# Performance work log

Hardware: AMD Instinct MI355X
Metric: run time of the kernel (lower is better)

Reference implementation:

```python
import jax, jax.numpy as jnp
import numpy as np

H = 2048          # hidden_size
IM = 1024         # moe_intermediate_size
E = 16            # n_routed_experts
K = 8             # num_experts_per_tok
N_SHARED = 2      # n_shared_experts
IS = IM * N_SHARED  # shared expert intermediate
B, L = 1, 2048
SCALE = 2.5       # routed_scaling_factor
W_INIT = 0.02


def setup_inputs() -> dict:
    key = jax.random.key(0)
    ks = jax.random.split(key, 9)
    return {
        "hidden_states": jax.random.normal(ks[0], (B, L, H), jnp.float32),
        "gate_w": jax.random.normal(ks[1], (E, H), jnp.float32) * W_INIT,
        "Wg": jax.random.normal(ks[2], (E, H, IM), jnp.float32) * W_INIT,
        "Wu": jax.random.normal(ks[3], (E, H, IM), jnp.float32) * W_INIT,
        "Wd": jax.random.normal(ks[4], (E, IM, H), jnp.float32) * W_INIT,
        "sWg": jax.random.normal(ks[5], (H, IS), jnp.float32) * W_INIT,
        "sWu": jax.random.normal(ks[6], (H, IS), jnp.float32) * W_INIT,
        "sWd": jax.random.normal(ks[7], (IS, H), jnp.float32) * W_INIT,
    }


def reference(hidden_states, gate_w, Wg, Wu, Wd, sWg, sWu, sWd):
    orig_shape = hidden_states.shape
    h = hidden_states.reshape(-1, H)                      # [T, H]
    T = h.shape[0]

    # shared expert (SwiGLU MLP)
    shared = (jax.nn.silu(h @ sWg) * (h @ sWu)) @ sWd     # [T, H]

    # sigmoid router + top-k gating
    router_logits = h @ gate_w.T                          # [T, E]
    routing_weights = jax.nn.sigmoid(router_logits)
    topk_w, topk_idx = jax.lax.top_k(routing_weights, K)  # [T, K]
    topk_w = topk_w / (jnp.sum(topk_w, axis=-1, keepdims=True) + 1e-6)
    topk_w = topk_w * SCALE

    # dense [T, E] combine weights (zero for unselected experts)
    comb = jnp.zeros((T, E), h.dtype).at[jnp.arange(T)[:, None], topk_idx].add(topk_w)

    # all-expert SwiGLU MLP (batched over experts), then weighted combine
    g = jnp.einsum("th,ehi->eti", h, Wg)                  # [E, T, IM]
    u = jnp.einsum("th,ehi->eti", h, Wu)
    eo = jnp.einsum("eti,eih->eth", jax.nn.silu(g) * u, Wd)  # [E, T, H]
    routed = jnp.einsum("eth,te->th", eo, comb)           # [T, H]

    return (shared + routed).reshape(orig_shape)
```

## Files before the change

kernel.cpp:

```cpp
#include <hip/hip_runtime.h>
#include <hip/hip_bf16.h>
#include <stdint.h>

#define H_DIM  2048
#define IM_DIM 1024
#define E_NUM  16
#define TOPK   8
#define IS_DIM 2048
#define SCALE_F 2.5f

#define BM 128
#define BN 128
#define BK 32
#define LDSP 40

typedef __attribute__((ext_vector_type(8))) short   short8;
typedef __attribute__((ext_vector_type(8))) __bf16  bf16x8;
typedef __attribute__((ext_vector_type(4))) float   float4v;
typedef unsigned short ushort_t;

#define GLOAD_LDS16(gp, lp) \
    __builtin_amdgcn_global_load_lds((__attribute__((address_space(1))) void*)(gp), \
                                     (__attribute__((address_space(3))) void*)(lp), 16, 0, 0)

static __device__ __forceinline__ ushort_t f2bf(float x) {
    union { float f; uint32_t u; } v; v.f = x;
    uint32_t r = v.u + 0x7fffu + ((v.u >> 16) & 1u);
    return (ushort_t)(r >> 16);
}

__global__ void cast_h_kernel(const float* __restrict__ h, ushort_t* __restrict__ hb, int n4) {
    int i = blockIdx.x * blockDim.x + threadIdx.x;
    if (i < n4) {
        float4 v = ((const float4*)h)[i];
        ushort4 o;
        o.x = f2bf(v.x); o.y = f2bf(v.y); o.z = f2bf(v.z); o.w = f2bf(v.w);
        ((ushort4*)hb)[i] = o;
    }
}

__global__ void router_kernel(const float* __restrict__ h, const float* __restrict__ gw,
                              float* __restrict__ comb, int T) {
    int t = blockIdx.x;
    int l = threadIdx.x;
    const float* hr = h + (size_t)t * H_DIM;
    __shared__ float logits[E_NUM];
    for (int e = 0; e < E_NUM; e++) {
        const float* g = gw + e * H_DIM;
        float p = 0.f;
        #pragma unroll 8
        for (int j = l; j < H_DIM; j += 64) p += hr[j] * g[j];
        #pragma unroll
        for (int off = 32; off > 0; off >>= 1) p += __shfl_down(p, off);
        if (l == 0) logits[e] = p;
    }
    __syncthreads();
    if (l == 0) {
        float sig[E_NUM]; bool sel[E_NUM];
        #pragma unroll
        for (int e = 0; e < E_NUM; e++) { sig[e] = 1.f / (1.f + expf(-logits[e])); sel[e] = false; }
        #pragma unroll
        for (int k = 0; k < TOPK; k++) {
            int bi = 0; float bv = -1.f;
            #pragma unroll
            for (int e = 0; e < E_NUM; e++)
                if (!sel[e] && sig[e] > bv) { bv = sig[e]; bi = e; }
            sel[bi] = true;
        }
        float s = 0.f;
        #pragma unroll
        for (int e = 0; e < E_NUM; e++) if (sel[e]) s += sig[e];
        float inv = SCALE_F / (s + 1e-6f);
        #pragma unroll
        for (int e = 0; e < E_NUM; e++)
            comb[(size_t)t * E_NUM + e] = sel[e] ? sig[e] * inv : 0.f;
    }
}

__global__ __launch_bounds__(256)
void transpose_cvt_kernel(const float* __restrict__ src, ushort_t* __restrict__ dst,
                          int K, int N, size_t sStride, size_t dStride)
{
    __shared__ float tile[64 * 65];
    int z = blockIdx.z;
    const float* S = src + (size_t)z * sStride;
    ushort_t* D = dst + (size_t)z * dStride;
    int k0 = blockIdx.x * 64, n0 = blockIdx.y * 64;
    int tid = threadIdx.x;
    int tr = tid >> 4, tc = (tid & 15) * 4;
    #pragma unroll
    for (int p = 0; p < 4; p++) {
        int r = tr + 16 * p;
        float4 v = *(const float4*)&S[(size_t)(k0 + r) * N + n0 + tc];
        tile[(tc + 0) * 65 + r] = v.x;
        tile[(tc + 1) * 65 + r] = v.y;
        tile[(tc + 2) * 65 + r] = v.z;
        tile[(tc + 3) * 65 + r] = v.w;
    }
    __syncthreads();
    #pragma unroll
    for (int p = 0; p < 4; p++) {
        int n = tr + 16 * p;
        ushort4 o;
        o.x = f2bf(tile[n * 65 + tc + 0]);
        o.y = f2bf(tile[n * 65 + tc + 1]);
        o.z = f2bf(tile[n * 65 + tc + 2]);
        o.w = f2bf(tile[n * 65 + tc + 3]);
        *(ushort4*)&D[(size_t)(n0 + n) * K + k0 + tc] = o;
    }
}


__global__ __launch_bounds__(256, 2)
void gemm1f_kernel(const ushort_t* __restrict__ A, int lda,
                   const ushort_t* __restrict__ Bg0, const ushort_t* __restrict__ Bu0,
                   size_t bSeg,
                   ushort_t* __restrict__ C0, size_t cSeg, int ldc,
                   const float* __restrict__ comb, int Kdim)
{
    __shared__ ushort_t Als[BM * BK];
    __shared__ ushort_t Bgs[BN * BK];
    __shared__ ushort_t Bus[BN * BK];

    int z = blockIdx.z;
    const ushort_t* Bg = Bg0 + (size_t)z * bSeg;
    const ushort_t* Bu = Bu0 + (size_t)z * bSeg;
    ushort_t* C = C0 + (size_t)z * cSeg;
    int t0 = blockIdx.x * BM, n0 = blockIdx.y * BN;
    int tid = threadIdx.x, lane = tid & 63, wid = tid >> 6;
    int wm = (wid & 1) * 64, wn = (wid >> 1) * 64;
    int quad = lane >> 4, l15 = lane & 15;

    int srow = lane >> 2;
    int scol = (lane & 3) * 8;
    int rb = wid * 32;

    float4v accg[4][4], accu[4][4];
    #pragma unroll
    for (int i = 0; i < 4; i++)
        #pragma unroll
        for (int j = 0; j < 4; j++) {
            accg[i][j] = (float4v){0.f, 0.f, 0.f, 0.f};
            accu[i][j] = (float4v){0.f, 0.f, 0.f, 0.f};
        }

    const ushort_t* Ab0  = A  + (size_t)(t0 + rb + srow)      * lda  + scol;
    const ushort_t* Ab1  = A  + (size_t)(t0 + rb + 16 + srow) * lda  + scol;
    const ushort_t* Bgb0 = Bg + (size_t)(n0 + rb + srow)      * Kdim + scol;
    const ushort_t* Bgb1 = Bg + (size_t)(n0 + rb + 16 + srow) * Kdim + scol;
    const ushort_t* Bub0 = Bu + (size_t)(n0 + rb + srow)      * Kdim + scol;
    const ushort_t* Bub1 = Bu + (size_t)(n0 + rb + 16 + srow) * Kdim + scol;
    ushort_t* lA0  = &Als[rb * BK];
    ushort_t* lA1  = &Als[(rb + 16) * BK];
    ushort_t* lBg0 = &Bgs[rb * BK];
    ushort_t* lBg1 = &Bgs[(rb + 16) * BK];
    ushort_t* lBu0 = &Bus[rb * BK];
    ushort_t* lBu1 = &Bus[(rb + 16) * BK];

    for (int k0 = 0; k0 < Kdim; k0 += BK) {
        GLOAD_LDS16(Ab0 + k0,  lA0);
        GLOAD_LDS16(Ab1 + k0,  lA1);
        GLOAD_LDS16(Bgb0 + k0, lBg0);
        GLOAD_LDS16(Bgb1 + k0, lBg1);
        GLOAD_LDS16(Bub0 + k0, lBu0);
        GLOAD_LDS16(Bub1 + k0, lBu1);
        __syncthreads();

        bf16x8 af[4], bg[4], bu[4];
        #pragma unroll
        for (int i = 0; i < 4; i++)
            af[i] = *(const bf16x8*)&Als[(wm + i * 16 + l15) * BK + quad * 8];
        #pragma unroll
        for (int j = 0; j < 4; j++) {
            bg[j] = *(const bf16x8*)&Bgs[(wn + j * 16 + l15) * BK + quad * 8];
            bu[j] = *(const bf16x8*)&Bus[(wn + j * 16 + l15) * BK + quad * 8];
        }
        #pragma unroll
        for (int i = 0; i < 4; i++)
            #pragma unroll
            for (int j = 0; j < 4; j++) {
                accg[i][j] = __builtin_amdgcn_mfma_f32_16x16x32_bf16(af[i], bg[j], accg[i][j], 0, 0, 0);
                accu[i][j] = __builtin_amdgcn_mfma_f32_16x16x32_bf16(af[i], bu[j], accu[i][j], 0, 0, 0);
            }
        __syncthreads();
    }

    #pragma unroll
    for (int i = 0; i < 4; i++) {
        #pragma unroll
        for (int r = 0; r < 4; r++) {
            int t = t0 + wm + i * 16 + quad * 4 + r;
            float sc = comb ? comb[(size_t)t * E_NUM + z] : 1.f;
            #pragma unroll
            for (int j = 0; j < 4; j++) {
                float g = accg[i][j][r], u = accu[i][j][r];
                float sg = g / (1.f + __expf(-g));
                float v = sg * u * sc;
                int c = n0 + wn + j * 16 + l15;
                C[(size_t)t * ldc + c] = f2bf(v);
            }
        }
    }
}

__global__ __launch_bounds__(256, 2)
void gemm2f_kernel(const ushort_t* __restrict__ A0, size_t aSeg, int lda,
                   const ushort_t* __restrict__ B0, size_t bSeg,
                   float* __restrict__ Out, int N,
                   int nsegPerZ, int Kper, int mode)
{
    __shared__ ushort_t Als[BM * BK];
    __shared__ ushort_t Bls[BN * BK];

    int t0 = blockIdx.x * BM, n0 = blockIdx.y * BN;
    int z = blockIdx.z;
    int tid = threadIdx.x, lane = tid & 63, wid = tid >> 6;
    int wm = (wid & 1) * 64, wn = (wid >> 1) * 64;
    int quad = lane >> 4, l15 = lane & 15;

    int srow = lane >> 2;
    int scol = (lane & 3) * 8;
    int rb = wid * 32;

    float4v acc[4][4];
    #pragma unroll
    for (int i = 0; i < 4; i++)
        #pragma unroll
        for (int j = 0; j < 4; j++) acc[i][j] = (float4v){0.f, 0.f, 0.f, 0.f};

    ushort_t* lA0 = &Als[rb * BK];
    ushort_t* lA1 = &Als[(rb + 16) * BK];
    ushort_t* lB0 = &Bls[rb * BK];
    ushort_t* lB1 = &Bls[(rb + 16) * BK];

    for (int s = 0; s < nsegPerZ; s++) {
        int seg = z * nsegPerZ + s;
        const ushort_t* A = A0 + (size_t)seg * aSeg;
        const ushort_t* B = B0 + (size_t)seg * bSeg;
        const ushort_t* Ab0 = A + (size_t)(t0 + rb + srow)      * lda  + scol;
        const ushort_t* Ab1 = A + (size_t)(t0 + rb + 16 + srow) * lda  + scol;
        const ushort_t* Bb0 = B + (size_t)(n0 + rb + srow)      * Kper + scol;
        const ushort_t* Bb1 = B + (size_t)(n0 + rb + 16 + srow) * Kper + scol;

        for (int k0 = 0; k0 < Kper; k0 += BK) {
            GLOAD_LDS16(Ab0 + k0, lA0);
            GLOAD_LDS16(Ab1 + k0, lA1);
            GLOAD_LDS16(Bb0 + k0, lB0);
            GLOAD_LDS16(Bb1 + k0, lB1);
            __syncthreads();

            bf16x8 af[4], bf[4];
            #pragma unroll
            for (int i = 0; i < 4; i++)
                af[i] = *(const bf16x8*)&Als[(wm + i * 16 + l15) * BK + quad * 8];
            #pragma unroll
            for (int j = 0; j < 4; j++)
                bf[j] = *(const bf16x8*)&Bls[(wn + j * 16 + l15) * BK + quad * 8];
            #pragma unroll
            for (int i = 0; i < 4; i++)
                #pragma unroll
                for (int j = 0; j < 4; j++)
                    acc[i][j] = __builtin_amdgcn_mfma_f32_16x16x32_bf16(af[i], bf[j], acc[i][j], 0, 0, 0);
            __syncthreads();
        }
    }

    #pragma unroll
    for (int i = 0; i < 4; i++) {
        #pragma unroll
        for (int r = 0; r < 4; r++) {
            int t = t0 + wm + i * 16 + quad * 4 + r;
            #pragma unroll
            for (int j = 0; j < 4; j++) {
                int c = n0 + wn + j * 16 + l15;
                size_t idx = (size_t)t * N + c;
                float v = acc[i][j][r];
                if (mode == 0) Out[idx] = v;
                else if (mode == 1) Out[idx] += v;
                else atomicAdd(&Out[idx], v);
            }
        }
    }
}


__global__ __launch_bounds__(256)
void gemm1_kernel(const ushort_t* __restrict__ A, int lda,
                  const float* __restrict__ Bg0, const float* __restrict__ Bu0,
                  size_t bSeg, int ldb,
                  ushort_t* __restrict__ C0, size_t cSeg, int ldc,
                  const float* __restrict__ comb, int Kdim)
{
    __shared__ ushort_t Als[BM * LDSP];
    __shared__ ushort_t Bgs[BN * LDSP];
    __shared__ ushort_t Bus[BN * LDSP];

    int z = blockIdx.z;
    const float* Bg = Bg0 + (size_t)z * bSeg;
    const float* Bu = Bu0 + (size_t)z * bSeg;
    ushort_t* C = C0 + (size_t)z * cSeg;

    int t0 = blockIdx.x * BM;
    int n0 = blockIdx.y * BN;
    int tid = threadIdx.x;
    int lane = tid & 63, wid = tid >> 6;
    int wm = (wid & 1) * 64, wn = (wid >> 1) * 64;
    int quad = lane >> 4, l15 = lane & 15;

    float4v accg[4][4], accu[4][4];
    #pragma unroll
    for (int i = 0; i < 4; i++)
        #pragma unroll
        for (int j = 0; j < 4; j++) {
            accg[i][j] = (float4v){0.f, 0.f, 0.f, 0.f};
            accu[i][j] = (float4v){0.f, 0.f, 0.f, 0.f};
        }

    int a_r  = tid >> 2, a_oc = tid & 3;
    int b_ko = (tid >> 4) & 3;
    int b_n  = 2 * ((tid & 15) + ((tid >> 6) << 4));

    for (int k0 = 0; k0 < Kdim; k0 += BK) {
        __syncthreads();
        {
            const ushort_t* s0 = A + (size_t)(t0 + a_r) * lda + k0 + a_oc * 8;
            *(short8*)&Als[a_r * LDSP + a_oc * 8] = *(const short8*)s0;
            const ushort_t* s1 = A + (size_t)(t0 + a_r + 64) * lda + k0 + a_oc * 8;
            *(short8*)&Als[(a_r + 64) * LDSP + a_oc * 8] = *(const short8*)s1;
        }
        {
            short8 g0, g1, u0, u1;
            #pragma unroll
            for (int j = 0; j < 8; j++) {
                size_t roff = (size_t)(k0 + b_ko * 8 + j) * ldb + n0 + b_n;
                float2 vg = *(const float2*)&Bg[roff];
                float2 vu = *(const float2*)&Bu[roff];
                g0[j] = (short)f2bf(vg.x); g1[j] = (short)f2bf(vg.y);
                u0[j] = (short)f2bf(vu.x); u1[j] = (short)f2bf(vu.y);
            }
            *(short8*)&Bgs[b_n * LDSP + b_ko * 8]       = g0;
            *(short8*)&Bgs[(b_n + 1) * LDSP + b_ko * 8] = g1;
            *(short8*)&Bus[b_n * LDSP + b_ko * 8]       = u0;
            *(short8*)&Bus[(b_n + 1) * LDSP + b_ko * 8] = u1;
        }
        __syncthreads();

        bf16x8 af[4], bg[4], bu[4];
        #pragma unroll
        for (int i = 0; i < 4; i++)
            af[i] = *(const bf16x8*)&Als[(wm + i * 16 + l15) * LDSP + quad * 8];
        #pragma unroll
        for (int j = 0; j < 4; j++) {
            bg[j] = *(const bf16x8*)&Bgs[(wn + j * 16 + l15) * LDSP + quad * 8];
            bu[j] = *(const bf16x8*)&Bus[(wn + j * 16 + l15) * LDSP + quad * 8];
        }
        #pragma unroll
        for (int i = 0; i < 4; i++)
            #pragma unroll
            for (int j = 0; j < 4; j++) {
                accg[i][j] = __builtin_amdgcn_mfma_f32_16x16x32_bf16(af[i], bg[j], accg[i][j], 0, 0, 0);
                accu[i][j] = __builtin_amdgcn_mfma_f32_16x16x32_bf16(af[i], bu[j], accu[i][j], 0, 0, 0);
            }
    }

    #pragma unroll
    for (int i = 0; i < 4; i++) {
        #pragma unroll
        for (int r = 0; r < 4; r++) {
            int t = t0 + wm + i * 16 + quad * 4 + r;
            float sc = comb ? comb[(size_t)t * E_NUM + z] : 1.f;
            #pragma unroll
            for (int j = 0; j < 4; j++) {
                float g = accg[i][j][r], u = accu[i][j][r];
                float sg = g / (1.f + __expf(-g));
                float v = sg * u * sc;
                int c = n0 + wn + j * 16 + l15;
                C[(size_t)t * ldc + c] = f2bf(v);
            }
        }
    }
}

__global__ __launch_bounds__(256)
void gemm2_kernel(const ushort_t* __restrict__ A0, size_t aSeg, int lda,
                  const float* __restrict__ B0, size_t bSeg, int ldb,
                  float* __restrict__ Out, int N,
                  int nseg, int Kper, int accum)
{
    __shared__ ushort_t Als[BM * LDSP];
    __shared__ ushort_t Bls[BN * LDSP];

    int t0 = blockIdx.x * BM;
    int n0 = blockIdx.y * BN;
    int tid = threadIdx.x;
    int lane = tid & 63, wid = tid >> 6;
    int wm = (wid & 1) * 64, wn = (wid >> 1) * 64;
    int quad = lane >> 4, l15 = lane & 15;

    float4v acc[4][4];
    #pragma unroll
    for (int i = 0; i < 4; i++)
        #pragma unroll
        for (int j = 0; j < 4; j++) acc[i][j] = (float4v){0.f, 0.f, 0.f, 0.f};

    int a_r  = tid >> 2, a_oc = tid & 3;
    int b_ko = (tid >> 4) & 3;
    int b_n  = 2 * ((tid & 15) + ((tid >> 6) << 4));

    for (int seg = 0; seg < nseg; seg++) {
        const ushort_t* A = A0 + (size_t)seg * aSeg;
        const float*    B = B0 + (size_t)seg * bSeg;
        for (int k0 = 0; k0 < Kper; k0 += BK) {
            __syncthreads();
            {
                const ushort_t* s0 = A + (size_t)(t0 + a_r) * lda + k0 + a_oc * 8;
                *(short8*)&Als[a_r * LDSP + a_oc * 8] = *(const short8*)s0;
                const ushort_t* s1 = A + (size_t)(t0 + a_r + 64) * lda + k0 + a_oc * 8;
                *(short8*)&Als[(a_r + 64) * LDSP + a_oc * 8] = *(const short8*)s1;
            }
            {
                short8 r0, r1;
                #pragma unroll
                for (int j = 0; j < 8; j++) {
                    size_t roff = (size_t)(k0 + b_ko * 8 + j) * ldb + n0 + b_n;
                    float2 v = *(const float2*)&B[roff];
                    r0[j] = (short)f2bf(v.x); r1[j] = (short)f2bf(v.y);
                }
                *(short8*)&Bls[b_n * LDSP + b_ko * 8]       = r0;
                *(short8*)&Bls[(b_n + 1) * LDSP + b_ko * 8] = r1;
            }
            __syncthreads();

            bf16x8 af[4], bf[4];
            #pragma unroll
            for (int i = 0; i < 4; i++)
                af[i] = *(const bf16x8*)&Als[(wm + i * 16 + l15) * LDSP + quad * 8];
            #pragma unroll
            for (int j = 0; j < 4; j++)
                bf[j] = *(const bf16x8*)&Bls[(wn + j * 16 + l15) * LDSP + quad * 8];
            #pragma unroll
            for (int i = 0; i < 4; i++)
                #pragma unroll
                for (int j = 0; j < 4; j++)
                    acc[i][j] = __builtin_amdgcn_mfma_f32_16x16x32_bf16(af[i], bf[j], acc[i][j], 0, 0, 0);
        }
    }

    #pragma unroll
    for (int i = 0; i < 4; i++) {
        #pragma unroll
        for (int r = 0; r < 4; r++) {
            int t = t0 + wm + i * 16 + quad * 4 + r;
            #pragma unroll
            for (int j = 0; j < 4; j++) {
                int c = n0 + wn + j * 16 + l15;
                size_t idx = (size_t)t * N + c;
                float v = acc[i][j][r];
                if (accum) Out[idx] += v; else Out[idx] = v;
            }
        }
    }
}


extern "C" void kernel_launch(void* const* d_in, const int* in_sizes, int n_in,
                              void* d_out, int out_size, void* d_ws, size_t ws_size,
                              hipStream_t stream) {
    const float* h      = (const float*)d_in[0];
    const float* gate_w = (const float*)d_in[1];
    const float* Wg     = (const float*)d_in[2];
    const float* Wu     = (const float*)d_in[3];
    const float* Wd     = (const float*)d_in[4];
    const float* sWg    = (const float*)d_in[5];
    const float* sWu    = (const float*)d_in[6];
    const float* sWd    = (const float*)d_in[7];
    float* out = (float*)d_out;
    int T = in_sizes[0] / H_DIM;
    (void)n_in; (void)out_size;

    char* ws = (char*)d_ws;
    size_t off = 0;
    auto alloc = [&](size_t bytes) -> void* {
        void* p = ws + off;
        off = (off + bytes + 255) & ~(size_t)255;
        return p;
    };
    ushort_t* h_bf  = (ushort_t*)alloc((size_t)T * H_DIM * 2);
    float*    comb  = (float*)   alloc((size_t)T * E_NUM * 4);
    ushort_t* act_s = (ushort_t*)alloc((size_t)T * IS_DIM * 2);
    ushort_t* act_r = (ushort_t*)alloc((size_t)E_NUM * T * IM_DIM * 2);
    ushort_t* bufS1 = (ushort_t*)alloc((size_t)IS_DIM * H_DIM * 2);
    ushort_t* bufS2 = (ushort_t*)alloc((size_t)IS_DIM * H_DIM * 2);
    ushort_t* bufW1 = (ushort_t*)alloc((size_t)E_NUM * IM_DIM * H_DIM * 2);
    ushort_t* bufW2 = (ushort_t*)alloc((size_t)E_NUM * IM_DIM * H_DIM * 2);
    size_t need = off;

    int n4 = T * H_DIM / 4;
    cast_h_kernel<<<(n4 + 255) / 256, 256, 0, stream>>>(h, h_bf, n4);
    router_kernel<<<T, 64, 0, stream>>>(h, gate_w, comb, T);

    if (ws_size >= need) {
        transpose_cvt_kernel<<<dim3(H_DIM / 64, IS_DIM / 64, 1), 256, 0, stream>>>(
            sWg, bufS1, H_DIM, IS_DIM, 0, 0);
        transpose_cvt_kernel<<<dim3(H_DIM / 64, IS_DIM / 64, 1), 256, 0, stream>>>(
            sWu, bufS2, H_DIM, IS_DIM, 0, 0);
        gemm1f_kernel<<<dim3(T / BM, IS_DIM / BN, 1), 256, 0, stream>>>(
            h_bf, H_DIM, bufS1, bufS2, 0, act_s, 0, IS_DIM, nullptr, H_DIM);

        transpose_cvt_kernel<<<dim3(H_DIM / 64, IM_DIM / 64, E_NUM), 256, 0, stream>>>(
            Wg, bufW1, H_DIM, IM_DIM, (size_t)H_DIM * IM_DIM, (size_t)IM_DIM * H_DIM);
        transpose_cvt_kernel<<<dim3(H_DIM / 64, IM_DIM / 64, E_NUM), 256, 0, stream>>>(
            Wu, bufW2, H_DIM, IM_DIM, (size_t)H_DIM * IM_DIM, (size_t)IM_DIM * H_DIM);
        gemm1f_kernel<<<dim3(T / BM, IM_DIM / BN, E_NUM), 256, 0, stream>>>(
            h_bf, H_DIM, bufW1, bufW2, (size_t)IM_DIM * H_DIM,
            act_r, (size_t)T * IM_DIM, IM_DIM, comb, H_DIM);

        transpose_cvt_kernel<<<dim3(IS_DIM / 64, H_DIM / 64, 1), 256, 0, stream>>>(
            sWd, bufS1, IS_DIM, H_DIM, 0, 0);
        gemm2f_kernel<<<dim3(T / BM, H_DIM / BN, 1), 256, 0, stream>>>(
            act_s, 0, IS_DIM, bufS1, 0, out, H_DIM, 1, IS_DIM, 0);

        transpose_cvt_kernel<<<dim3(IM_DIM / 64, H_DIM / 64, E_NUM), 256, 0, stream>>>(
            Wd, bufW1, IM_DIM, H_DIM, (size_t)IM_DIM * H_DIM, (size_t)H_DIM * IM_DIM);
        gemm2f_kernel<<<dim3(T / BM, H_DIM / BN, 2), 256, 0, stream>>>(
            act_r, (size_t)T * IM_DIM, IM_DIM, bufW1, (size_t)H_DIM * IM_DIM,
            out, H_DIM, E_NUM / 2, IM_DIM, 2);
    } else {
        gemm1_kernel<<<dim3(T / BM, IS_DIM / BN, 1), 256, 0, stream>>>(
            h_bf, H_DIM, sWg, sWu, 0, IS_DIM, act_s, 0, IS_DIM, nullptr, H_DIM);
        gemm1_kernel<<<dim3(T / BM, IM_DIM / BN, E_NUM), 256, 0, stream>>>(
            h_bf, H_DIM, Wg, Wu, (size_t)H_DIM * IM_DIM, IM_DIM,
            act_r, (size_t)T * IM_DIM, IM_DIM, comb, H_DIM);
        gemm2_kernel<<<dim3(T / BM, H_DIM / BN, 1), 256, 0, stream>>>(
            act_s, 0, IS_DIM, sWd, 0, H_DIM, out, H_DIM, 1, IS_DIM, 0);
        gemm2_kernel<<<dim3(T / BM, H_DIM / BN, 1), 256, 0, stream>>>(
            act_r, (size_t)T * IM_DIM, IM_DIM, Wd, (size_t)IM_DIM * H_DIM, H_DIM,
            out, H_DIM, E_NUM, IM_DIM, 1);
    }
}
```

Before: 1.149 ms.

## Replace dense all-expert MoE GEMMs with sparse gathered per-expert token lists

```diff
diff --git a/kernel.cpp b/kernel.cpp
--- a/kernel.cpp
+++ b/kernel.cpp
@@ -77,6 +77,37 @@
     }
 }
 
+__global__ void zero_cnt_kernel(int* __restrict__ cnt) {
+    if (threadIdx.x < E_NUM) cnt[threadIdx.x] = 0;
+}
+
+__global__ void build_lists_kernel(const float* __restrict__ comb, int* __restrict__ cnt,
+                                   int* __restrict__ idx, float* __restrict__ wv, int T) {
+    int t = blockIdx.x * blockDim.x + threadIdx.x;
+    if (t >= T) return;
+    #pragma unroll
+    for (int e = 0; e < E_NUM; e++) {
+        float w = comb[(size_t)t * E_NUM + e];
+        if (w != 0.f) {
+            int s = atomicAdd(&cnt[e], 1);
+            idx[(size_t)e * T + s] = t;
+            wv[(size_t)e * T + s] = w;
+        }
+    }
+}
+
+__global__ void pad_lists_kernel(const int* __restrict__ cnt, int* __restrict__ cntPad,
+                                 int* __restrict__ idx, float* __restrict__ wv, int T) {
+    int e = blockIdx.x;
+    int c = cnt[e];
+    int cp = (c + BM - 1) & ~(BM - 1);
+    if (threadIdx.x == 0) cntPad[e] = cp;
+    for (int s = c + threadIdx.x; s < cp; s += blockDim.x) {
+        idx[(size_t)e * T + s] = 0;
+        wv[(size_t)e * T + s] = 0.f;
+    }
+}
+
 __global__ __launch_bounds__(256)
 void transpose_cvt_kernel(const float* __restrict__ src, ushort_t* __restrict__ dst,
                           int K, int N, size_t sStride, size_t dStride)
@@ -113,27 +144,18 @@
 
 __global__ __launch_bounds__(256, 2)
 void gemm1f_kernel(const ushort_t* __restrict__ A, int lda,
-                   const ushort_t* __restrict__ Bg0, const ushort_t* __restrict__ Bu0,
-                   size_t bSeg,
-                   ushort_t* __restrict__ C0, size_t cSeg, int ldc,
-                   const float* __restrict__ comb, int Kdim)
+                   const ushort_t* __restrict__ Bg, const ushort_t* __restrict__ Bu,
+                   ushort_t* __restrict__ C, int ldc, int Kdim)
 {
     __shared__ ushort_t Als[BM * BK];
     __shared__ ushort_t Bgs[BN * BK];
     __shared__ ushort_t Bus[BN * BK];
 
-    int z = blockIdx.z;
-    const ushort_t* Bg = Bg0 + (size_t)z * bSeg;
-    const ushort_t* Bu = Bu0 + (size_t)z * bSeg;
-    ushort_t* C = C0 + (size_t)z * cSeg;
     int t0 = blockIdx.x * BM, n0 = blockIdx.y * BN;
     int tid = threadIdx.x, lane = tid & 63, wid = tid >> 6;
     int wm = (wid & 1) * 64, wn = (wid >> 1) * 64;
     int quad = lane >> 4, l15 = lane & 15;
-
-    int srow = lane >> 2;
-    int scol = (lane & 3) * 8;
-    int rb = wid * 32;
+    int srow = lane >> 2, scol = (lane & 3) * 8, rb = wid * 32;
 
     float4v accg[4][4], accu[4][4];
     #pragma unroll
@@ -190,37 +212,30 @@
         #pragma unroll
         for (int r = 0; r < 4; r++) {
             int t = t0 + wm + i * 16 + quad * 4 + r;
-            float sc = comb ? comb[(size_t)t * E_NUM + z] : 1.f;
             #pragma unroll
             for (int j = 0; j < 4; j++) {
                 float g = accg[i][j][r], u = accu[i][j][r];
                 float sg = g / (1.f + __expf(-g));
-                float v = sg * u * sc;
                 int c = n0 + wn + j * 16 + l15;
-                C[(size_t)t * ldc + c] = f2bf(v);
+                C[(size_t)t * ldc + c] = f2bf(sg * u);
             }
         }
     }
 }
 
 __global__ __launch_bounds__(256, 2)
-void gemm2f_kernel(const ushort_t* __restrict__ A0, size_t aSeg, int lda,
-                   const ushort_t* __restrict__ B0, size_t bSeg,
-                   float* __restrict__ Out, int N,
-                   int nsegPerZ, int Kper, int mode)
+void gemm2f_kernel(const ushort_t* __restrict__ A, int lda,
+                   const ushort_t* __restrict__ B,
+                   float* __restrict__ Out, int N, int Kper)
 {
     __shared__ ushort_t Als[BM * BK];
     __shared__ ushort_t Bls[BN * BK];
 
     int t0 = blockIdx.x * BM, n0 = blockIdx.y * BN;
-    int z = blockIdx.z;
     int tid = threadIdx.x, lane = tid & 63, wid = tid >> 6;
     int wm = (wid & 1) * 64, wn = (wid >> 1) * 64;
     int quad = lane >> 4, l15 = lane & 15;
-
-    int srow = lane >> 2;
-    int scol = (lane & 3) * 8;
-    int rb = wid * 32;
+    int srow = lane >> 2, scol = (lane & 3) * 8, rb = wid * 32;
 
     float4v acc[4][4];
     #pragma unroll
@@ -228,41 +243,35 @@
         #pragma unroll
         for (int j = 0; j < 4; j++) acc[i][j] = (float4v){0.f, 0.f, 0.f, 0.f};
 
+    const ushort_t* Ab0 = A + (size_t)(t0 + rb + srow)      * lda  + scol;
+    const ushort_t* Ab1 = A + (size_t)(t0 + rb + 16 + srow) * lda  + scol;
+    const ushort_t* Bb0 = B + (size_t)(n0 + rb + srow)      * Kper + scol;
+    const ushort_t* Bb1 = B + (size_t)(n0 + rb + 16 + srow) * Kper + scol;
     ushort_t* lA0 = &Als[rb * BK];
     ushort_t* lA1 = &Als[(rb + 16) * BK];
     ushort_t* lB0 = &Bls[rb * BK];
     ushort_t* lB1 = &Bls[(rb + 16) * BK];
 
-    for (int s = 0; s < nsegPerZ; s++) {
-        int seg = z * nsegPerZ + s;
-        const ushort_t* A = A0 + (size_t)seg * aSeg;
-        const ushort_t* B = B0 + (size_t)seg * bSeg;
-        const ushort_t* Ab0 = A + (size_t)(t0 + rb + srow)      * lda  + scol;
-        const ushort_t* Ab1 = A + (size_t)(t0 + rb + 16 + srow) * lda  + scol;
-        const ushort_t* Bb0 = B + (size_t)(n0 + rb + srow)      * Kper + scol;
-        const ushort_t* Bb1 = B + (size_t)(n0 + rb + 16 + srow) * Kper + scol;
-
-        for (int k0 = 0; k0 < Kper; k0 += BK) {
-            GLOAD_LDS16(Ab0 + k0, lA0);
-            GLOAD_LDS16(Ab1 + k0, lA1);
-            GLOAD_LDS16(Bb0 + k0, lB0);
-            GLOAD_LDS16(Bb1 + k0, lB1);
-            __syncthreads();
-
-            bf16x8 af[4], bf[4];
-            #pragma unroll
-            for (int i = 0; i < 4; i++)
-                af[i] = *(const bf16x8*)&Als[(wm + i * 16 + l15) * BK + quad * 8];
+    for (int k0 = 0; k0 < Kper; k0 += BK) {
+        GLOAD_LDS16(Ab0 + k0, lA0);
+        GLOAD_LDS16(Ab1 + k0, lA1);
+        GLOAD_LDS16(Bb0 + k0, lB0);
+        GLOAD_LDS16(Bb1 + k0, lB1);
+        __syncthreads();
+
+        bf16x8 af[4], bf[4];
+        #pragma unroll
+        for (int i = 0; i < 4; i++)
+            af[i] = *(const bf16x8*)&Als[(wm + i * 16 + l15) * BK + quad * 8];
+        #pragma unroll
+        for (int j = 0; j < 4; j++)
+            bf[j] = *(const bf16x8*)&Bls[(wn + j * 16 + l15) * BK + quad * 8];
+        #pragma unroll
+        for (int i = 0; i < 4; i++)
             #pragma unroll
             for (int j = 0; j < 4; j++)
-                bf[j] = *(const bf16x8*)&Bls[(wn + j * 16 + l15) * BK + quad * 8];
-            #pragma unroll
-            for (int i = 0; i < 4; i++)
-                #pragma unroll
-                for (int j = 0; j < 4; j++)
-                    acc[i][j] = __builtin_amdgcn_mfma_f32_16x16x32_bf16(af[i], bf[j], acc[i][j], 0, 0, 0);
-            __syncthreads();
-        }
+                acc[i][j] = __builtin_amdgcn_mfma_f32_16x16x32_bf16(af[i], bf[j], acc[i][j], 0, 0, 0);
+        __syncthreads();
     }
 
     #pragma unroll
@@ -273,11 +282,179 @@
             #pragma unroll
             for (int j = 0; j < 4; j++) {
                 int c = n0 + wn + j * 16 + l15;
-                size_t idx = (size_t)t * N + c;
-                float v = acc[i][j][r];
-                if (mode == 0) Out[idx] = v;
-                else if (mode == 1) Out[idx] += v;
-                else atomicAdd(&Out[idx], v);
+                Out[(size_t)t * N + c] = acc[i][j][r];
+            }
+        }
+    }
+}
+
+
+__global__ __launch_bounds__(256, 2)
+void gemm1s_kernel(const ushort_t* __restrict__ hb,
+                   const ushort_t* __restrict__ BgT0, const ushort_t* __restrict__ BuT0,
+                   const int* __restrict__ idx, const float* __restrict__ wv,
+                   const int* __restrict__ cntPad,
+                   ushort_t* __restrict__ actC, int T)
+{
+    int e = blockIdx.z;
+    int m0 = blockIdx.x * BM;
+    if (m0 >= cntPad[e]) return;
+    int n0 = blockIdx.y * BN;
+
+    const ushort_t* Bg = BgT0 + (size_t)e * IM_DIM * H_DIM;
+    const ushort_t* Bu = BuT0 + (size_t)e * IM_DIM * H_DIM;
+    const int* idxE = idx + (size_t)e * T;
+    const float* wvE = wv + (size_t)e * T;
+    ushort_t* C = actC + (size_t)e * T * IM_DIM;
+
+    int tid = threadIdx.x, lane = tid & 63, wid = tid >> 6;
+    int wm = (wid & 1) * 64, wn = (wid >> 1) * 64;
+    int quad = lane >> 4, l15 = lane & 15;
+    int srow = lane >> 2, scol = (lane & 3) * 8, rb = wid * 32;
+
+    __shared__ ushort_t Als[BM * BK];
+    __shared__ ushort_t Bgs[BN * BK];
+    __shared__ ushort_t Bus[BN * BK];
+
+    float4v accg[4][4], accu[4][4];
+    #pragma unroll
+    for (int i = 0; i < 4; i++)
+        #pragma unroll
+        for (int j = 0; j < 4; j++) {
+            accg[i][j] = (float4v){0.f, 0.f, 0.f, 0.f};
+            accu[i][j] = (float4v){0.f, 0.f, 0.f, 0.f};
+        }
+
+    int tI0 = idxE[m0 + rb + srow];
+    int tI1 = idxE[m0 + rb + 16 + srow];
+    const ushort_t* Ab0  = hb + (size_t)tI0 * H_DIM + scol;
+    const ushort_t* Ab1  = hb + (size_t)tI1 * H_DIM + scol;
+    const ushort_t* Bgb0 = Bg + (size_t)(n0 + rb + srow)      * H_DIM + scol;
+    const ushort_t* Bgb1 = Bg + (size_t)(n0 + rb + 16 + srow) * H_DIM + scol;
+    const ushort_t* Bub0 = Bu + (size_t)(n0 + rb + srow)      * H_DIM + scol;
+    const ushort_t* Bub1 = Bu + (size_t)(n0 + rb + 16 + srow) * H_DIM + scol;
+    ushort_t* lA0  = &Als[rb * BK];
+    ushort_t* lA1  = &Als[(rb + 16) * BK];
+    ushort_t* lBg0 = &Bgs[rb * BK];
+    ushort_t* lBg1 = &Bgs[(rb + 16) * BK];
+    ushort_t* lBu0 = &Bus[rb * BK];
+    ushort_t* lBu1 = &Bus[(rb + 16) * BK];
+
+    for (int k0 = 0; k0 < H_DIM; k0 += BK) {
+        GLOAD_LDS16(Ab0 + k0,  lA0);
+        GLOAD_LDS16(Ab1 + k0,  lA1);
+        GLOAD_LDS16(Bgb0 + k0, lBg0);
+        GLOAD_LDS16(Bgb1 + k0, lBg1);
+        GLOAD_LDS16(Bub0 + k0, lBu0);
+        GLOAD_LDS16(Bub1 + k0, lBu1);
+        __syncthreads();
+
+        bf16x8 af[4], bg[4], bu[4];
+        #pragma unroll
+        for (int i = 0; i < 4; i++)
+            af[i] = *(const bf16x8*)&Als[(wm + i * 16 + l15) * BK + quad * 8];
+        #pragma unroll
+        for (int j = 0; j < 4; j++) {
+            bg[j] = *(const bf16x8*)&Bgs[(wn + j * 16 + l15) * BK + quad * 8];
+            bu[j] = *(const bf16x8*)&Bus[(wn + j * 16 + l15) * BK + quad * 8];
+        }
+        #pragma unroll
+        for (int i = 0; i < 4; i++)
+            #pragma unroll
+            for (int j = 0; j < 4; j++) {
+                accg[i][j] = __builtin_amdgcn_mfma_f32_16x16x32_bf16(af[i], bg[j], accg[i][j], 0, 0, 0);
+                accu[i][j] = __builtin_amdgcn_mfma_f32_16x16x32_bf16(af[i], bu[j], accu[i][j], 0, 0, 0);
+            }
+        __syncthreads();
+    }
+
+    #pragma unroll
+    for (int i = 0; i < 4; i++) {
+        #pragma unroll
+        for (int r = 0; r < 4; r++) {
+            int slot = m0 + wm + i * 16 + quad * 4 + r;
+            float sc = wvE[slot];
+            #pragma unroll
+            for (int j = 0; j < 4; j++) {
+                float g = accg[i][j][r], u = accu[i][j][r];
+                float sg = g / (1.f + __expf(-g));
+                int c = n0 + wn + j * 16 + l15;
+                C[(size_t)slot * IM_DIM + c] = f2bf(sg * u * sc);
+            }
+        }
+    }
+}
+
+__global__ __launch_bounds__(256, 2)
+void gemm2s_kernel(const ushort_t* __restrict__ actC,
+                   const ushort_t* __restrict__ WdT0,
+                   const int* __restrict__ idx, const int* __restrict__ cntPad,
+                   float* __restrict__ Out, int T)
+{
+    int e = blockIdx.z;
+    int m0 = blockIdx.x * BM;
+    if (m0 >= cntPad[e]) return;
+    int n0 = blockIdx.y * BN;
+
+    const ushort_t* A = actC + (size_t)e * T * IM_DIM;
+    const ushort_t* B = WdT0 + (size_t)e * H_DIM * IM_DIM;
+    const int* idxE = idx + (size_t)e * T;
+
+    int tid = threadIdx.x, lane = tid & 63, wid = tid >> 6;
+    int wm = (wid & 1) * 64, wn = (wid >> 1) * 64;
+    int quad = lane >> 4, l15 = lane & 15;
+    int srow = lane >> 2, scol = (lane & 3) * 8, rb = wid * 32;
+
+    __shared__ ushort_t Als[BM * BK];
+    __shared__ ushort_t Bls[BN * BK];
+
+    float4v acc[4][4];
+    #pragma unroll
+    for (int i = 0; i < 4; i++)
+        #pragma unroll
+        for (int j = 0; j < 4; j++) acc[i][j] = (float4v){0.f, 0.f, 0.f, 0.f};
+
+    const ushort_t* Ab0 = A + (size_t)(m0 + rb + srow)      * IM_DIM + scol;
+    const ushort_t* Ab1 = A + (size_t)(m0 + rb + 16 + srow) * IM_DIM + scol;
+    const ushort_t* Bb0 = B + (size_t)(n0 + rb + srow)      * IM_DIM + scol;
+    const ushort_t* Bb1 = B + (size_t)(n0 + rb + 16 + srow) * IM_DIM + scol;
+    ushort_t* lA0 = &Als[rb * BK];
+    ushort_t* lA1 = &Als[(rb + 16) * BK];
+    ushort_t* lB0 = &Bls[rb * BK];
+    ushort_t* lB1 = &Bls[(rb + 16) * BK];
+
+    for (int k0 = 0; k0 < IM_DIM; k0 += BK) {
+        GLOAD_LDS16(Ab0 + k0, lA0);
+        GLOAD_LDS16(Ab1 + k0, lA1);
+        GLOAD_LDS16(Bb0 + k0, lB0);
+        GLOAD_LDS16(Bb1 + k0, lB1);
+        __syncthreads();
+
+        bf16x8 af[4], bf[4];
+        #pragma unroll
+        for (int i = 0; i < 4; i++)
+            af[i] = *(const bf16x8*)&Als[(wm + i * 16 + l15) * BK + quad * 8];
+        #pragma unroll
+        for (int j = 0; j < 4; j++)
+            bf[j] = *(const bf16x8*)&Bls[(wn + j * 16 + l15) * BK + quad * 8];
+        #pragma unroll
+        for (int i = 0; i < 4; i++)
+            #pragma unroll
+            for (int j = 0; j < 4; j++)
+                acc[i][j] = __builtin_amdgcn_mfma_f32_16x16x32_bf16(af[i], bf[j], acc[i][j], 0, 0, 0);
+        __syncthreads();
+    }
+
+    #pragma unroll
+    for (int i = 0; i < 4; i++) {
+        #pragma unroll
+        for (int r = 0; r < 4; r++) {
+            int slot = m0 + wm + i * 16 + quad * 4 + r;
+            int t = idxE[slot];
+            #pragma unroll
+            for (int j = 0; j < 4; j++) {
+                int c = n0 + wn + j * 16 + l15;
+                atomicAdd(&Out[(size_t)t * H_DIM + c], acc[i][j][r]);
             }
         }
     }
@@ -488,7 +665,11 @@
     ushort_t* h_bf  = (ushort_t*)alloc((size_t)T * H_DIM * 2);
     float*    comb  = (float*)   alloc((size_t)T * E_NUM * 4);
     ushort_t* act_s = (ushort_t*)alloc((size_t)T * IS_DIM * 2);
-    ushort_t* act_r = (ushort_t*)alloc((size_t)E_NUM * T * IM_DIM * 2);
+    ushort_t* act_c = (ushort_t*)alloc((size_t)E_NUM * T * IM_DIM * 2);
+    int*      eidx  = (int*)     alloc((size_t)E_NUM * T * 4);
+    float*    ewv   = (float*)   alloc((size_t)E_NUM * T * 4);
+    int*      cnt   = (int*)     alloc(E_NUM * 4);
+    int*      cntP  = (int*)     alloc(E_NUM * 4);
     ushort_t* bufS1 = (ushort_t*)alloc((size_t)IS_DIM * H_DIM * 2);
     ushort_t* bufS2 = (ushort_t*)alloc((size_t)IS_DIM * H_DIM * 2);
     ushort_t* bufW1 = (ushort_t*)alloc((size_t)E_NUM * IM_DIM * H_DIM * 2);
@@ -500,41 +681,43 @@
     router_kernel<<<T, 64, 0, stream>>>(h, gate_w, comb, T);
 
     if (ws_size >= need) {
+        zero_cnt_kernel<<<1, 64, 0, stream>>>(cnt);
+        build_lists_kernel<<<(T + 255) / 256, 256, 0, stream>>>(comb, cnt, eidx, ewv, T);
+        pad_lists_kernel<<<E_NUM, 128, 0, stream>>>(cnt, cntP, eidx, ewv, T);
+
         transpose_cvt_kernel<<<dim3(H_DIM / 64, IS_DIM / 64, 1), 256, 0, stream>>>(
             sWg, bufS1, H_DIM, IS_DIM, 0, 0);
         transpose_cvt_kernel<<<dim3(H_DIM / 64, IS_DIM / 64, 1), 256, 0, stream>>>(
             sWu, bufS2, H_DIM, IS_DIM, 0, 0);
         gemm1f_kernel<<<dim3(T / BM, IS_DIM / BN, 1), 256, 0, stream>>>(
-            h_bf, H_DIM, bufS1, bufS2, 0, act_s, 0, IS_DIM, nullptr, H_DIM);
+            h_bf, H_DIM, bufS1, bufS2, act_s, IS_DIM, H_DIM);
 
         transpose_cvt_kernel<<<dim3(H_DIM / 64, IM_DIM / 64, E_NUM), 256, 0, stream>>>(
             Wg, bufW1, H_DIM, IM_DIM, (size_t)H_DIM * IM_DIM, (size_t)IM_DIM * H_DIM);
         transpose_cvt_kernel<<<dim3(H_DIM / 64, IM_DIM / 64, E_NUM), 256, 0, stream>>>(
             Wu, bufW2, H_DIM, IM_DIM, (size_t)H_DIM * IM_DIM, (size_t)IM_DIM * H_DIM);
-        gemm1f_kernel<<<dim3(T / BM, IM_DIM / BN, E_NUM), 256, 0, stream>>>(
-            h_bf, H_DIM, bufW1, bufW2, (size_t)IM_DIM * H_DIM,
-            act_r, (size_t)T * IM_DIM, IM_DIM, comb, H_DIM);
+        gemm1s_kernel<<<dim3(T / BM, IM_DIM / BN, E_NUM), 256, 0, stream>>>(
+            h_bf, bufW1, bufW2, eidx, ewv, cntP, act_c, T);
 
         transpose_cvt_kernel<<<dim3(IS_DIM / 64, H_DIM / 64, 1), 256, 0, stream>>>(
             sWd, bufS1, IS_DIM, H_DIM, 0, 0);
         gemm2f_kernel<<<dim3(T / BM, H_DIM / BN, 1), 256, 0, stream>>>(
-            act_s, 0, IS_DIM, bufS1, 0, out, H_DIM, 1, IS_DIM, 0);
+            act_s, IS_DIM, bufS1, out, H_DIM, IS_DIM);
 
         transpose_cvt_kernel<<<dim3(IM_DIM / 64, H_DIM / 64, E_NUM), 256, 0, stream>>>(
             Wd, bufW1, IM_DIM, H_DIM, (size_t)IM_DIM * H_DIM, (size_t)H_DIM * IM_DIM);
-        gemm2f_kernel<<<dim3(T / BM, H_DIM / BN, 2), 256, 0, stream>>>(
-            act_r, (size_t)T * IM_DIM, IM_DIM, bufW1, (size_t)H_DIM * IM_DIM,
-            out, H_DIM, E_NUM / 2, IM_DIM, 2);
+        gemm2s_kernel<<<dim3(T / BM, H_DIM / BN, E_NUM), 256, 0, stream>>>(
+            act_c, bufW1, eidx, cntP, out, T);
     } else {
         gemm1_kernel<<<dim3(T / BM, IS_DIM / BN, 1), 256, 0, stream>>>(
             h_bf, H_DIM, sWg, sWu, 0, IS_DIM, act_s, 0, IS_DIM, nullptr, H_DIM);
         gemm1_kernel<<<dim3(T / BM, IM_DIM / BN, E_NUM), 256, 0, stream>>>(
             h_bf, H_DIM, Wg, Wu, (size_t)H_DIM * IM_DIM, IM_DIM,
-            act_r, (size_t)T * IM_DIM, IM_DIM, comb, H_DIM);
+            act_c, (size_t)T * IM_DIM, IM_DIM, comb, H_DIM);
         gemm2_kernel<<<dim3(T / BM, H_DIM / BN, 1), 256, 0, stream>>>(
             act_s, 0, IS_DIM, sWd, 0, H_DIM, out, H_DIM, 1, IS_DIM, 0);
         gemm2_kernel<<<dim3(T / BM, H_DIM / BN, 1), 256, 0, stream>>>(
-            act_r, (size_t)T * IM_DIM, IM_DIM, Wd, (size_t)IM_DIM * H_DIM, H_DIM,
+            act_c, (size_t)T * IM_DIM, IM_DIM, Wd, (size_t)IM_DIM * H_DIM, H_DIM,
             out, H_DIM, E_NUM, IM_DIM, 1);
     }
 }
```

Measured after the change: 1.173 ms. 2.1% more time.
